# Performance work log

Hardware: AMD Instinct MI355X
Metric: run time of the kernel (lower is better)

Reference implementation:

```python
import jax, jax.numpy as jnp
import numpy as np

N_FEATURES = 512
DEPTH = 6
N_TREES = 64
D_OUT = 64
N_LEAVES = 2 ** DEPTH


def setup_inputs() -> dict:
    key = jax.random.key(0)
    k_x, k_w, k_b, k_leaf = jax.random.split(key, 4)
    B = 16384
    x = jax.random.normal(k_x, (B, N_FEATURES), dtype=jnp.float32)
    # depth independent Linear(n_features, n_trees) layers, stacked
    bound = 1.0 / np.sqrt(N_FEATURES)
    W = jax.random.uniform(k_w, (DEPTH, N_FEATURES, N_TREES), dtype=jnp.float32,
                           minval=-bound, maxval=bound)
    b = jax.random.uniform(k_b, (DEPTH, N_TREES), dtype=jnp.float32,
                           minval=-bound, maxval=bound)
    leaf_values = jax.random.normal(k_leaf, (N_TREES, N_LEAVES, D_OUT), dtype=jnp.float32)
    return {"x": x, "W": W, "b": b, "leaf_values": leaf_values}


def reference(x, W, b, leaf_values):
    B = x.shape[0]
    # split probabilities for all levels at once: [B, depth, n_trees]
    split_probs = jax.nn.sigmoid(jnp.einsum('bf,dft->bdt', x, W) + b)
    # bit of leaf index at each level: 0 -> take p (left), 1 -> take 1-p (right)
    leaf_ids = jnp.arange(N_LEAVES)
    # path_probs: [B, n_trees, n_leaves]; small fixed loop over depth levels
    path_probs = jnp.ones((B, N_TREES, N_LEAVES), dtype=x.dtype)
    for level in range(DEPTH):
        bit = (leaf_ids >> (DEPTH - level - 1)) & 1  # [n_leaves]
        p = split_probs[:, level, :, None]           # [B, n_trees, 1]
        path_probs = path_probs * jnp.where(bit == 0, p, 1.0 - p)
    # per-tree leaf combine then mean over trees
    out = jnp.einsum('btl,tld->bd', path_probs, leaf_values) / N_TREES
    return out
```

## Files before the change

### kernel.cpp

```cpp
#include <hip/hip_runtime.h>

#define BATCH   16384
#define NFEAT   512
#define NTREE   64
#define NDEPTH  6
#define NLEAF   64
#define NDOUT   64
#define NLOGIT  384

typedef float    f32x4  __attribute__((ext_vector_type(4)));
typedef short    short8 __attribute__((ext_vector_type(8)));
typedef _Float16 half8  __attribute__((ext_vector_type(8)));
typedef _Float16 h2     __attribute__((ext_vector_type(2)));

union U8 { unsigned short u[8]; short8 v; half8 h; };
union HP { _Float16 h[4]; ushort4 u; };
union HS { _Float16 h; unsigned short s; };
union H8 { h2 p[4]; half8 v; };

__device__ __forceinline__ unsigned short f2bf(float f) {
    union { float f; unsigned int u; } c; c.f = f;
    return (unsigned short)((c.u + 0x8000u) >> 16);
}

__device__ __forceinline__ unsigned short f2h(float f) {
    HS s; s.h = (_Float16)f; return s.s;
}

__device__ __forceinline__ void dma16(const void* g, void* l) {
    __builtin_amdgcn_global_load_lds(
        (const __attribute__((address_space(1))) unsigned int*)g,
        (__attribute__((address_space(3))) unsigned int*)l, 16, 0, 0);
}

__global__ __launch_bounds__(256) void prep(const float* __restrict__ leaf,
                                            const float* __restrict__ W,
                                            unsigned short* __restrict__ V3,
                                            unsigned short* __restrict__ Wt3) {
    __shared__ float T[64 * 65];
    const int tid = threadIdx.x;
    if (blockIdx.x < 64) {
        const int t = blockIdx.x;
        const float* src = leaf + (size_t)t * 4096;
        for (int j = 0; j < 4; ++j) {
            int idx = tid + 256 * j;
            int l = idx >> 4, d4 = idx & 15;
            float4 v = *(const float4*)(src + l * 64 + d4 * 4);
            T[l * 65 + d4 * 4 + 0] = v.x;
            T[l * 65 + d4 * 4 + 1] = v.y;
            T[l * 65 + d4 * 4 + 2] = v.z;
            T[l * 65 + d4 * 4 + 3] = v.w;
        }
        __syncthreads();
        #pragma unroll
        for (int jj = 0; jj < 2; ++jj) {
            int idx = tid + 256 * jj;
            int d = idx >> 3, o = idx & 7;
            int nt = d >> 4, l15 = d & 15;
            int ks = o >> 2, qd = o & 3;
            int lam = qd * 16 + l15;
            U8 u;
            #pragma unroll
            for (int j = 0; j < 8; ++j)
                u.u[j] = f2h(T[(o * 8 + j) * 65 + d] * 0.015625f);
            *(short8*)(V3 + (((size_t)t * 8 + nt * 2 + ks) * 64 + lam) * 8) = u.v;
        }
    } else {
        const int bid = blockIdx.x - 64;
        const int d = bid >> 4, f0 = (bid & 15) * 32;
        for (int j = 0; j < 2; ++j) {
            int idx = tid + 256 * j;
            int f = idx >> 4, c4 = idx & 15;
            float4 v = *(const float4*)(W + ((size_t)d * 512 + f0 + f) * 64 + c4 * 4);
            T[f * 65 + c4 * 4 + 0] = v.x;
            T[f * 65 + c4 * 4 + 1] = v.y;
            T[f * 65 + c4 * 4 + 2] = v.z;
            T[f * 65 + c4 * 4 + 3] = v.w;
        }
        __syncthreads();
        const int t = tid >> 2, c8 = tid & 3;
        U8 u;
        #pragma unroll
        for (int i = 0; i < 8; ++i) u.u[i] = f2bf(T[(c8 * 8 + i) * 65 + t]);
        int k0 = f0 + c8 * 8;
        int kb = k0 >> 6, ks = (k0 >> 5) & 1, qk = (k0 >> 3) & 3;
        int g  = d * 4 + (t >> 4);
        int lam = qk * 16 + (t & 15);
        *(short8*)(Wt3 + (((size_t)kb * 24 + g) * 2 + ks) * 512 + lam * 8) = u.v;
    }
}

__global__ __launch_bounds__(256) void fused(const float* __restrict__ x,
                                             const unsigned short* __restrict__ Wt3,
                                             const float* __restrict__ bias,
                                             const unsigned short* __restrict__ V3,
                                             float* __restrict__ out) {
    __shared__ char SM[44 * 1024];
    _Float16*       sp  = (_Float16*)SM;
    float*          As0 = (float*)(SM + 24 * 1024);
    float*          As1 = (float*)(SM + 32 * 1024);
    _Float16*       red = (_Float16*)(SM + 24 * 1024);

    const int tid  = threadIdx.x;
    const int w = tid >> 6, lane = tid & 63;
    const int quad = lane >> 4, l15 = lane & 15;
    const int r0 = blockIdx.x * 32;
    const int w6 = w * 6;

    f32x4 acc1[2][6];
    #pragma unroll
    for (int mt = 0; mt < 2; ++mt)
        #pragma unroll
        for (int nt = 0; nt < 6; ++nt)
            acc1[mt][nt] = (f32x4){0.f, 0.f, 0.f, 0.f};

    auto stageA = [&](float* buf, int kb) {
        #pragma unroll
        for (int i = 0; i < 2; ++i) {
            int j  = w * 2 + i;
            int rl = j * 4 + (lane >> 4);
            const float* g = x + (size_t)(r0 + rl) * NFEAT + kb * 64
                           + (((lane & 15) ^ ((rl & 7) * 2)) * 4);
            dma16(g, (char*)buf + (size_t)j * 1024);
        }
    };
    auto loadBF = [&](int kb, short8 (*bf)[2]) {
        #pragma unroll
        for (int nt = 0; nt < 6; ++nt)
            #pragma unroll
            for (int ks = 0; ks < 2; ++ks)
                bf[nt][ks] = *(const short8*)(Wt3 +
                    (((size_t)kb * 24 + w6 + nt) * 2 + ks) * 512 + lane * 8);
    };
    auto computeStep = [&](const float* buf, short8 (*bf)[2]) {
        short8 aF[2][2];
        #pragma unroll
        for (int mt = 0; mt < 2; ++mt) {
            int r = mt * 16 + l15;
            #pragma unroll
            for (int ks = 0; ks < 2; ++ks) {
                int cb = (ks * 8 + quad * 2) ^ ((r & 7) * 2);
                float4 f0 = *(const float4*)(buf + r * 64 + cb * 4);
                float4 f1 = *(const float4*)(buf + r * 64 + cb * 4 + 4);
                U8 u;
                u.u[0] = f2bf(f0.x); u.u[1] = f2bf(f0.y);
                u.u[2] = f2bf(f0.z); u.u[3] = f2bf(f0.w);
                u.u[4] = f2bf(f1.x); u.u[5] = f2bf(f1.y);
                u.u[6] = f2bf(f1.z); u.u[7] = f2bf(f1.w);
                aF[mt][ks] = u.v;
            }
        }
        #pragma unroll
        for (int mt = 0; mt < 2; ++mt)
            #pragma unroll
            for (int nt = 0; nt < 6; ++nt)
                #pragma unroll
                for (int ks = 0; ks < 2; ++ks)
                    acc1[mt][nt] = __builtin_amdgcn_mfma_f32_16x16x32_bf16(
                        aF[mt][ks], bf[nt][ks], acc1[mt][nt], 0, 0, 0);
    };

    short8 bC[6][2], bN[6][2];
    stageA(As0, 0);
    loadBF(0, bC);
    __syncthreads();
    #pragma unroll
    for (int kp = 0; kp < 4; ++kp) {
        int kb = kp * 2;
        stageA(As1, kb + 1);
        loadBF(kb + 1, bN);
        computeStep(As0, bC);
        __syncthreads();
        if (kb + 2 < 8) {
            stageA(As0, kb + 2);
            loadBF(kb + 2, bC);
        }
        computeStep(As1, bN);
        __syncthreads();
    }

    #pragma unroll
    for (int nt = 0; nt < 6; ++nt) {
        int n = w * 96 + nt * 16 + l15;
        float bv = bias[n];
        #pragma unroll
        for (int mt = 0; mt < 2; ++mt) {
            HP h;
            #pragma unroll
            for (int r = 0; r < 4; ++r) {
                float z = acc1[mt][nt][r] + bv;
                h.h[r] = (_Float16)(1.0f / (1.0f + __expf(-z)));
            }
            *(ushort4*)(sp + n * 32 + mt * 16 + quad * 4) = h.u;
        }
    }
    __syncthreads();

    const _Float16* V3h = (const _Float16*)V3;

    f32x4 acc[2][4];
    #pragma unroll
    for (int mt = 0; mt < 2; ++mt)
        #pragma unroll
        for (int nt = 0; nt < 4; ++nt)
            acc[mt][nt] = (f32x4){0.f, 0.f, 0.f, 0.f};

    auto loadB = [&](int t, half8 (*bf)[2]) {
        #pragma unroll
        for (int nt = 0; nt < 4; ++nt)
            #pragma unroll
            for (int ks = 0; ks < 2; ++ks)
                bf[nt][ks] = *(const half8*)(V3h +
                    (((size_t)t * 8 + nt * 2 + ks) * 64 + lane) * 8);
    };
    auto buildA = [&](int t, half8 (*af)[2]) {
        const _Float16 one = (_Float16)1.0f;
        #pragma unroll
        for (int mt = 0; mt < 2; ++mt) {
            int rl = mt * 16 + l15;
            _Float16 p0 = sp[(0 * 64 + t) * 32 + rl];
            _Float16 p1 = sp[(1 * 64 + t) * 32 + rl];
            _Float16 p2 = sp[(2 * 64 + t) * 32 + rl];
            _Float16 p3 = sp[(3 * 64 + t) * 32 + rl];
            _Float16 p4 = sp[(4 * 64 + t) * 32 + rl];
            _Float16 p5 = sp[(5 * 64 + t) * 32 + rl];
            _Float16 q1 = (quad & 2) ? (_Float16)(one - p1) : p1;
            _Float16 q2 = (quad & 1) ? (_Float16)(one - p2) : p2;
            _Float16 pre  = q1 * q2;
            _Float16 pre0 = p0 * pre;
            _Float16 pre1 = (_Float16)(one - p0) * pre;
            h2 t45 = { p4, (_Float16)(one - p4) };
            h2 t5  = { p5, (_Float16)(one - p5) };
            h2 a34 = (h2){ p3, p3 } * t45;
            _Float16 q3 = one - p3;
            h2 b34 = (h2){ q3, q3 } * t45;
            h2 w0 = (h2){ a34.x, a34.x } * t5;
            h2 w1 = (h2){ a34.y, a34.y } * t5;
            h2 w2 = (h2){ b34.x, b34.x } * t5;
            h2 w3 = (h2){ b34.y, b34.y } * t5;
            h2 P0 = { pre0, pre0 }, P1 = { pre1, pre1 };
            H8 a0, a1;
            a0.p[0] = P0 * w0; a0.p[1] = P0 * w1;
            a0.p[2] = P0 * w2; a0.p[3] = P0 * w3;
            a1.p[0] = P1 * w0; a1.p[1] = P1 * w1;
            a1.p[2] = P1 * w2; a1.p[3] = P1 * w3;
            af[mt][0] = a0.v;
            af[mt][1] = a1.v;
        }
    };

    half8 bA[4][2], bB[4][2], aF2[2][2];
    loadB(w * 16, bA);
    #pragma unroll 2
    for (int tl = 0; tl < 16; ++tl) {
        const int t = w * 16 + tl;
        half8 (*cur)[2] = (tl & 1) ? bB : bA;
        half8 (*nxt)[2] = (tl & 1) ? bA : bB;
        if (tl + 1 < 16) loadB(t + 1, nxt);
        buildA(t, aF2);
        #pragma unroll
        for (int mt = 0; mt < 2; ++mt)
            #pragma unroll
            for (int nt = 0; nt < 4; ++nt)
                #pragma unroll
                for (int ks = 0; ks < 2; ++ks)
                    acc[mt][nt] = __builtin_amdgcn_mfma_f32_16x16x32_f16(
                        aF2[mt][ks], cur[nt][ks], acc[mt][nt], 0, 0, 0);
    }

    #pragma unroll
    for (int mt = 0; mt < 2; ++mt)
        #pragma unroll
        for (int nt = 0; nt < 4; ++nt) {
            HP h;
            #pragma unroll
            for (int r = 0; r < 4; ++r) h.h[r] = (_Float16)acc[mt][nt][r];
            *(ushort4*)(red + (w * 64 + nt * 16 + l15) * 40 + mt * 16 + quad * 4) = h.u;
        }
    __syncthreads();
    {
        int b = tid >> 3;
        int doff = (tid & 7) * 8;
        float s[8];
        #pragma unroll
        for (int i = 0; i < 8; ++i) s[i] = 0.f;
        #pragma unroll
        for (int ww = 0; ww < 4; ++ww)
            #pragma unroll
            for (int i = 0; i < 8; ++i)
                s[i] += (float)red[(ww * 64 + doff + i) * 40 + b];
        float4 o0 = { s[0], s[1], s[2], s[3] };
        float4 o1 = { s[4], s[5], s[6], s[7] };
        float* dst = out + (size_t)(r0 + b) * NDOUT + doff;
        *(float4*)dst = o0;
        *(float4*)(dst + 4) = o1;
    }
}

extern "C" void kernel_launch(void* const* d_in, const int* in_sizes, int n_in,
                              void* d_out, int out_size, void* d_ws, size_t ws_size,
                              hipStream_t stream) {
    const float* x    = (const float*)d_in[0];
    const float* W    = (const float*)d_in[1];
    const float* bias = (const float*)d_in[2];
    const float* leaf = (const float*)d_in[3];
    float* out = (float*)d_out;

    unsigned short* V3  = (unsigned short*)d_ws;
    unsigned short* Wt3 = V3 + (size_t)NTREE * NLEAF * NDOUT;

    prep<<<160, 256, 0, stream>>>(leaf, W, V3, Wt3);
    fused<<<BATCH / 32, 256, 0, stream>>>(x, Wt3, bias, (const unsigned short*)V3, out);
}
```

Baseline: 100.2 us.

## Load x fragments directly from global instead of LDS double-buffered DMA staging

Removes the global-to-LDS DMA staging of x tiles and the explicit double-buffered software pipeline with its barriers. Each wave now reads its A fragments straight from global memory into registers and loads the B fragments inside a simple loop unrolled by two. This drops LDS traffic and per-step __syncthreads, but leaves latency hiding to the compiler. The four waves now load the same x rows redundantly from global/L2, and the 32-byte-per-lane row accesses coalesce less well.

```diff
diff --git a/kernel.cpp b/kernel.cpp
--- a/kernel.cpp
+++ b/kernel.cpp
@@ -25,12 +25,6 @@
 
 __device__ __forceinline__ unsigned short f2h(float f) {
     HS s; s.h = (_Float16)f; return s.s;
-}
-
-__device__ __forceinline__ void dma16(const void* g, void* l) {
-    __builtin_amdgcn_global_load_lds(
-        (const __attribute__((address_space(1))) unsigned int*)g,
-        (__attribute__((address_space(3))) unsigned int*)l, 16, 0, 0);
 }
 
 __global__ __launch_bounds__(256) void prep(const float* __restrict__ leaf,
@@ -97,8 +91,6 @@
                                              float* __restrict__ out) {
     __shared__ char SM[44 * 1024];
     _Float16*       sp  = (_Float16*)SM;
-    float*          As0 = (float*)(SM + 24 * 1024);
-    float*          As1 = (float*)(SM + 32 * 1024);
     _Float16*       red = (_Float16*)(SM + 24 * 1024);
 
     const int tid  = threadIdx.x;
@@ -114,34 +106,17 @@
         for (int nt = 0; nt < 6; ++nt)
             acc1[mt][nt] = (f32x4){0.f, 0.f, 0.f, 0.f};
 
-    auto stageA = [&](float* buf, int kb) {
-        #pragma unroll
-        for (int i = 0; i < 2; ++i) {
-            int j  = w * 2 + i;
-            int rl = j * 4 + (lane >> 4);
-            const float* g = x + (size_t)(r0 + rl) * NFEAT + kb * 64
-                           + (((lane & 15) ^ ((rl & 7) * 2)) * 4);
-            dma16(g, (char*)buf + (size_t)j * 1024);
-        }
-    };
-    auto loadBF = [&](int kb, short8 (*bf)[2]) {
-        #pragma unroll
-        for (int nt = 0; nt < 6; ++nt)
-            #pragma unroll
-            for (int ks = 0; ks < 2; ++ks)
-                bf[nt][ks] = *(const short8*)(Wt3 +
-                    (((size_t)kb * 24 + w6 + nt) * 2 + ks) * 512 + lane * 8);
-    };
-    auto computeStep = [&](const float* buf, short8 (*bf)[2]) {
+    #pragma unroll 2
+    for (int kb = 0; kb < 8; ++kb) {
         short8 aF[2][2];
         #pragma unroll
         for (int mt = 0; mt < 2; ++mt) {
-            int r = mt * 16 + l15;
             #pragma unroll
             for (int ks = 0; ks < 2; ++ks) {
-                int cb = (ks * 8 + quad * 2) ^ ((r & 7) * 2);
-                float4 f0 = *(const float4*)(buf + r * 64 + cb * 4);
-                float4 f1 = *(const float4*)(buf + r * 64 + cb * 4 + 4);
+                const float* g = x + (size_t)(r0 + mt * 16 + l15) * NFEAT
+                               + kb * 64 + ks * 32 + quad * 8;
+                float4 f0 = *(const float4*)(g);
+                float4 f1 = *(const float4*)(g + 4);
                 U8 u;
                 u.u[0] = f2bf(f0.x); u.u[1] = f2bf(f0.y);
                 u.u[2] = f2bf(f0.z); u.u[3] = f2bf(f0.w);
@@ -150,6 +125,13 @@
                 aF[mt][ks] = u.v;
             }
         }
+        short8 bF[6][2];
+        #pragma unroll
+        for (int nt = 0; nt < 6; ++nt)
+            #pragma unroll
+            for (int ks = 0; ks < 2; ++ks)
+                bF[nt][ks] = *(const short8*)(Wt3 +
+                    (((size_t)kb * 24 + w6 + nt) * 2 + ks) * 512 + lane * 8);
         #pragma unroll
         for (int mt = 0; mt < 2; ++mt)
             #pragma unroll
@@ -157,26 +139,7 @@
                 #pragma unroll
                 for (int ks = 0; ks < 2; ++ks)
                     acc1[mt][nt] = __builtin_amdgcn_mfma_f32_16x16x32_bf16(
-                        aF[mt][ks], bf[nt][ks], acc1[mt][nt], 0, 0, 0);
-    };
-
-    short8 bC[6][2], bN[6][2];
-    stageA(As0, 0);
-    loadBF(0, bC);
-    __syncthreads();
-    #pragma unroll
-    for (int kp = 0; kp < 4; ++kp) {
-        int kb = kp * 2;
-        stageA(As1, kb + 1);
-        loadBF(kb + 1, bN);
-        computeStep(As0, bC);
-        __syncthreads();
-        if (kb + 2 < 8) {
-            stageA(As0, kb + 2);
-            loadBF(kb + 2, bC);
-        }
-        computeStep(As1, bN);
-        __syncthreads();
+                        aF[mt][ks], bF[nt][ks], acc1[mt][nt], 0, 0, 0);
     }
 
     #pragma unroll
```

Result: slower. 110.1 us (+9.8%).
